# Optimization experiments

Measured on AMD Instinct MI355X. Metric: run time of the kernel, lower is better.

The kernel has to match this reference:

```python
import jax, jax.numpy as jnp
import numpy as np

B, L, S, E, H = 2, 2048, 2048, 1024, 16
D = E // H


def setup_inputs() -> dict:
    key = jax.random.key(0)
    ks = jax.random.split(key, 16)
    p = 0.02  # small init scale for weights
    return {
        "a": jax.random.normal(ks[0], (B, L, E), jnp.float32),
        "b": jax.random.normal(ks[1], (B, S, E), jnp.float32),
        "Wa_qk": jax.random.normal(ks[2], (E, E), jnp.float32) * p,
        "ba_qk": jax.random.normal(ks[3], (E,), jnp.float32) * p,
        "Wa_v": jax.random.normal(ks[4], (E, E), jnp.float32) * p,
        "ba_v": jax.random.normal(ks[5], (E,), jnp.float32) * p,
        "Wb_qk": jax.random.normal(ks[6], (E, E), jnp.float32) * p,
        "bb_qk": jax.random.normal(ks[7], (E,), jnp.float32) * p,
        "Wb_v": jax.random.normal(ks[8], (E, E), jnp.float32) * p,
        "bb_v": jax.random.normal(ks[9], (E,), jnp.float32) * p,
        "Wa_o": jax.random.normal(ks[10], (E, E), jnp.float32) * p,
        "ba_o": jax.random.normal(ks[11], (E,), jnp.float32) * p,
        "Wb_o": jax.random.normal(ks[12], (E, E), jnp.float32) * p,
        "bb_o": jax.random.normal(ks[13], (E,), jnp.float32) * p,
    }


def _heads(x, n, W, bias):
    # x: [B, N, E] -> projected and split to [B, H, N, D]
    y = x @ W + bias
    return y.reshape(B, n, H, D).transpose(0, 2, 1, 3)


def reference(a, b, Wa_qk, ba_qk, Wa_v, ba_v, Wb_qk, bb_qk, Wb_v, bb_v,
              Wa_o, ba_o, Wb_o, bb_o):
    aq = _heads(a, L, Wa_qk, ba_qk)   # [B,H,L,D]
    av = _heads(a, L, Wa_v, ba_v)     # [B,H,L,D]
    bq = _heads(b, S, Wb_qk, bb_qk)   # [B,H,S,D]
    bv = _heads(b, S, Wb_v, bb_v)     # [B,H,S,D]

    scale = 1.0 / jnp.sqrt(jnp.float32(D))
    # Shared score matrix [B,H,L,S]
    scores = jnp.einsum('bhld,bhsd->bhls', aq, bq) * scale
    # Dual softmax: row-wise (over S) and column-wise (over L)
    wa = jax.nn.softmax(scores, axis=-1)                    # [B,H,L,S]
    wb = jax.nn.softmax(scores, axis=-2).transpose(0, 1, 3, 2)  # [B,H,S,L]

    a_ctx = jnp.einsum('bhls,bhsd->bhld', wa, bv)  # [B,H,L,D]
    b_ctx = jnp.einsum('bhsl,bhld->bhsd', wb, av)  # [B,H,S,D]

    a_out = a_ctx.transpose(0, 2, 1, 3).reshape(B, L, E) @ Wa_o + ba_o
    b_out = b_ctx.transpose(0, 2, 1, 3).reshape(B, S, E) @ Wb_o + bb_o
    return (a_out, b_out)
```

## Files before the change

### kernel.cpp

```cpp
#include <hip/hip_runtime.h>
#include <hip/hip_bf16.h>
#include <stdint.h>

typedef unsigned short u16;
typedef unsigned int u32;
typedef __attribute__((ext_vector_type(8))) short bf16x8;
typedef __attribute__((ext_vector_type(4))) float f32x4;

typedef __attribute__((address_space(3))) void lds_void;
typedef const __attribute__((address_space(1))) void gbl_void;

#define SIDE 4194304u
#define BHSTR 131072u

static __device__ __forceinline__ u16 f2bf(float f) {
  union { __hip_bfloat16 b; u16 u; } cv;
  cv.b = __float2bfloat16(f);
  return cv.u;
}
static __device__ __forceinline__ float bf2f(u16 u) {
  union { __hip_bfloat16 b; u16 u; } cv;
  cv.u = u;
  return __bfloat162float(cv.b);
}

static __device__ __forceinline__ void pl16swap(u32& a, u32& b) {
#if __has_builtin(__builtin_amdgcn_permlane16_swap)
  typedef __attribute__((ext_vector_type(2))) unsigned int u32x2;
  u32x2 r = __builtin_amdgcn_permlane16_swap(a, b, 0, 0);
  a = r[0];
  b = r[1];
#else
  asm volatile("v_permlane16_swap_b32 %0, %1" : "+v"(a), "+v"(b));
#endif
}

__global__ __launch_bounds__(256) void k_cvt_in(const float* __restrict__ a,
                                                const float* __restrict__ b,
                                                u16* __restrict__ dst) {
  int z = blockIdx.y;
  const float* src = z ? b : a;
  size_t i = ((size_t)blockIdx.x * 256 + threadIdx.x) * 8;
  float4 x0 = *(const float4*)(src + i);
  float4 x1 = *(const float4*)(src + i + 4);
  u16 t[8] = {f2bf(x0.x), f2bf(x0.y), f2bf(x0.z), f2bf(x0.w),
              f2bf(x1.x), f2bf(x1.y), f2bf(x1.z), f2bf(x1.w)};
  *(uint4*)(dst + (size_t)z * SIDE + i) = *(uint4*)t;
}

__global__ __launch_bounds__(256) void k_cvt_bias(
    const float* s0, const float* s1, const float* s2, const float* s3,
    const float* s4, const float* s5, u16* __restrict__ dst) {
  const float* srcs[6] = {s0, s1, s2, s3, s4, s5};
  int z = blockIdx.y;
  int i = blockIdx.x * 256 + threadIdx.x;
  float sc = (z == 0) ? 0.18033688011112042f : 1.0f;
  dst[z * 1024 + i] = f2bf(srcs[z][i] * sc);
}

__global__ __launch_bounds__(256) void k_transpose_w(
    const float* a0, const float* a1, const float* a2, const float* a3,
    const float* a4, const float* a5,
    u16* d0, u16* d1, u16* d2, u16* d3, u16* d4, u16* d5) {
  __shared__ u16 tile[64][72];
  const float* srcs[6] = {a0, a1, a2, a3, a4, a5};
  u16* dsts[6] = {d0, d1, d2, d3, d4, d5};
  int z = blockIdx.z;
  float sc = (z == 0) ? 0.18033688011112042f : 1.0f;
  const float* src = srcs[z] + (size_t)(blockIdx.y * 64) * 1024 + blockIdx.x * 64;
  int t = threadIdx.x;
  int row = t >> 2, c4 = t & 3;
#pragma unroll
  for (int p = 0; p < 2; ++p) {
    int col = c4 * 8 + p * 32;
    const float* sf = src + (size_t)row * 1024 + col;
    float4 x0 = *(const float4*)sf;
    float4 x1 = *(const float4*)(sf + 4);
    u16 tmp[8] = {f2bf(x0.x * sc), f2bf(x0.y * sc), f2bf(x0.z * sc), f2bf(x0.w * sc),
                  f2bf(x1.x * sc), f2bf(x1.y * sc), f2bf(x1.z * sc), f2bf(x1.w * sc)};
    *(uint4*)(&tile[row][col]) = *(uint4*)tmp;
  }
  __syncthreads();
  u16* dst = dsts[z] + (size_t)(blockIdx.x * 64) * 1024 + blockIdx.y * 64;
#pragma unroll
  for (int p = 0; p < 2; ++p) {
    int col = c4 * 8 + p * 32;
    u16 tmp[8];
#pragma unroll
    for (int i = 0; i < 8; ++i) tmp[i] = tile[col + i][row];
    *(uint4*)(dst + (size_t)row * 1024 + col) = *(uint4*)tmp;
  }
}

__global__ __launch_bounds__(256) void k_gemm_qkv(
    const u16* __restrict__ Aall, const u16* __restrict__ WtA,
    const u16* __restrict__ WtB, const u16* __restrict__ bias,
    u16* __restrict__ qkbuf, u16* __restrict__ vbuf) {
  __shared__ u16 Sh[8192];
  u16* As = Sh;
  u16* Bs = Sh + 4096;
  int tid = threadIdx.x;
  int wave = tid >> 6, lane = tid & 63;
  int quad = lane >> 4, lrow = lane & 15;
  int wr = wave >> 1, wc = wave & 1;
  int z = blockIdx.z;
  int m0 = blockIdx.y * 128, n0 = blockIdx.x * 128;
  const u16* A = Aall + (size_t)z * SIDE;
  const u16* Wt = z ? WtB : WtA;
  const u16* bi = bias + (size_t)z * 2048;

  f32x4 acc[4][4] = {};
  int srow = 32 * wave + (lane >> 2);
  int scol = (lane & 3) * 8;
  const u16* gA = A + (size_t)(m0 + srow) * 1024 + scol;
  const u16* gB = Wt + (size_t)(n0 + srow) * 1024 + scol;
  u16* lA = &As[(32 * wave) * 32];
  u16* lB = &Bs[(32 * wave) * 32];

  for (int k0 = 0; k0 < 1024; k0 += 32) {
    __syncthreads();
#pragma unroll
    for (int j = 0; j < 2; ++j) {
      __builtin_amdgcn_global_load_lds((gbl_void*)(gA + (size_t)(16 * j) * 1024 + k0),
                                       (lds_void*)(lA + 16 * j * 32), 16, 0, 0);
      __builtin_amdgcn_global_load_lds((gbl_void*)(gB + (size_t)(16 * j) * 1024 + k0),
                                       (lds_void*)(lB + 16 * j * 32), 16, 0, 0);
    }
    __syncthreads();
    bf16x8 af[4], bfr[4];
#pragma unroll
    for (int i = 0; i < 4; ++i)
      af[i] = *(const bf16x8*)&As[(64 * wr + 16 * i + lrow) * 32 + 8 * quad];
#pragma unroll
    for (int j = 0; j < 4; ++j)
      bfr[j] = *(const bf16x8*)&Bs[(64 * wc + 16 * j + lrow) * 32 + 8 * quad];
#pragma unroll
    for (int i = 0; i < 4; ++i)
#pragma unroll
      for (int j = 0; j < 4; ++j)
        acc[i][j] = __builtin_amdgcn_mfma_f32_16x16x32_bf16(af[i], bfr[j], acc[i][j], 0, 0, 0);
  }

  float bv[4];
#pragma unroll
  for (int j = 0; j < 4; ++j) bv[j] = bf2f(bi[n0 + 64 * wc + 16 * j + lrow]);

  int x = blockIdx.x;
  bool isv = (x >= 8);
  int h = (isv ? 2 * (x - 8) : 2 * x) + wc;
  u16* dst = (isv ? vbuf : qkbuf) + (size_t)z * SIDE;
  u16* lw = Sh + wave * 1216;

  __syncthreads();
#pragma unroll
  for (int i = 0; i < 4; ++i) {
#pragma unroll
    for (int j = 0; j < 4; ++j)
#pragma unroll
      for (int r = 0; r < 4; ++r)
        lw[(4 * quad + r) * 76 + 16 * j + lrow] = f2bf(acc[i][j][r] + bv[j]);
    asm volatile("s_waitcnt lgkmcnt(0)" ::: "memory");
    int row = lane >> 2, cg = (lane & 3) * 16;
    int rg = m0 + 64 * wr + 16 * i + row;
    int bb = rg >> 11, rl = rg & 2047;
    u16* dr = dst + (size_t)(bb * 16 + h) * BHSTR + (size_t)rl * 64 + cg;
    uint2 w0 = *(const uint2*)&lw[row * 76 + cg];
    uint2 w1 = *(const uint2*)&lw[row * 76 + cg + 4];
    uint2 w2 = *(const uint2*)&lw[row * 76 + cg + 8];
    uint2 w3 = *(const uint2*)&lw[row * 76 + cg + 12];
    uint4 o0 = {w0.x, w0.y, w1.x, w1.y};
    uint4 o1 = {w2.x, w2.y, w3.x, w3.y};
    *(uint4*)dr = o0;
    *(uint4*)(dr + 8) = o1;
    asm volatile("s_waitcnt lgkmcnt(0)" ::: "memory");
  }
}

__global__ __launch_bounds__(256) void k_transpose_v(const u16* __restrict__ v,
                                                     u16* __restrict__ vt) {
  __shared__ u16 tile[64][72];
  int sbh = blockIdx.y;
  int n0 = blockIdx.x * 64;
  const u16* src = v + (size_t)sbh * BHSTR + (size_t)n0 * 64;
  u16* dst = vt + (size_t)sbh * BHSTR + n0;
  int t = threadIdx.x;
  int row = t >> 2, c4 = t & 3;
#pragma unroll
  for (int p = 0; p < 2; ++p) {
    int col = c4 * 8 + p * 32;
    uint4 q = *(const uint4*)(src + (size_t)row * 64 + col);
    *(uint4*)(&tile[row][col]) = q;
  }
  __syncthreads();
#pragma unroll
  for (int p = 0; p < 2; ++p) {
    int col = c4 * 8 + p * 32;
    u16 tmp[8];
#pragma unroll
    for (int i = 0; i < 8; ++i) tmp[i] = tile[col + i][row];
    *(uint4*)(dst + (size_t)row * 2048 + col) = *(uint4*)tmp;
  }
}

__global__ __launch_bounds__(256, 4) void k_attn(
    const u16* __restrict__ qk, const u16* __restrict__ vt,
    u16* __restrict__ ctx) {
  __shared__ u16 Ks[2 * 4096];
  __shared__ u16 Vs[2 * 4096];
  int tid = threadIdx.x;
  int wave = tid >> 6, lane = tid & 63;
  int quad = lane >> 4, lrow = lane & 15;
  int z = blockIdx.z, bh = blockIdx.x;
  int l0 = blockIdx.y * 128;
  const u16* Qb = qk + (size_t)z * SIDE + (size_t)bh * BHSTR + (size_t)l0 * 64;
  const u16* Kb = qk + (size_t)(1 - z) * SIDE + (size_t)bh * BHSTR;
  const u16* Vtb = vt + (size_t)(1 - z) * SIDE + (size_t)bh * BHSTR;

  bf16x8 qf[2][2];
#pragma unroll
  for (int rt = 0; rt < 2; ++rt) {
    int lq = 32 * wave + 16 * rt + lrow;
    qf[rt][0] = *(const bf16x8*)&Qb[(size_t)lq * 64 + 8 * quad];
    qf[rt][1] = *(const bf16x8*)&Qb[(size_t)lq * 64 + 32 + 8 * quad];
  }

  int r0 = tid >> 3, c0 = tid & 7;
  int r1 = (256 + tid) >> 3;
  const u16* kS0 = Kb + (size_t)r0 * 64 + ((c0 ^ (r0 & 7)) * 8);
  const u16* kS1 = Kb + (size_t)r1 * 64 + ((c0 ^ (r1 & 7)) * 8);
  const u16* vS0 = Vtb + (size_t)r0 * 2048 + ((c0 ^ (r0 & 7)) * 8);
  const u16* vS1 = Vtb + (size_t)r1 * 2048 + ((c0 ^ (r1 & 7)) * 8);
  u16* kD0 = Ks + (wave * 64) * 8;
  u16* kD1 = Ks + (256 + wave * 64) * 8;
  u16* vD0 = Vs + (wave * 64) * 8;
  u16* vD1 = Vs + (256 + wave * 64) * 8;

  bf16x8 ones;
  {
    short o = 0x3F80;
#pragma unroll
    for (int i = 0; i < 8; ++i) ones[i] = o;
  }

  f32x4 cacc[2][4] = {};
  f32x4 asum[2] = {};
  int gsq = 2 * (quad & 1) + (quad >> 1);

#define STAGE(BUFOFF, IT)                                                        \
  __builtin_amdgcn_global_load_lds((gbl_void*)(kS0 + (size_t)(IT)*4096),         \
                                   (lds_void*)(kD0 + (BUFOFF)), 16, 0, 0);       \
  __builtin_amdgcn_global_load_lds((gbl_void*)(kS1 + (size_t)(IT)*4096),         \
                                   (lds_void*)(kD1 + (BUFOFF)), 16, 0, 0);       \
  __builtin_amdgcn_global_load_lds((gbl_void*)(vS0 + (size_t)(IT)*64),           \
                                   (lds_void*)(vD0 + (BUFOFF)), 16, 0, 0);       \
  __builtin_amdgcn_global_load_lds((gbl_void*)(vS1 + (size_t)(IT)*64),           \
                                   (lds_void*)(vD1 + (BUFOFF)), 16, 0, 0);

#define ATT_BODY(BUFOFF)                                                         \
  {                                                                              \
    const u16* KsC = Ks + (BUFOFF);                                              \
    const u16* VsC = Vs + (BUFOFF);                                              \
    u32 X[2][4], Y[2][4];                                                        \
    _Pragma("unroll") for (int j = 0; j < 4; ++j) {                              \
      int kr = 16 * j + lrow;                                                    \
      bf16x8 kf0 = *(const bf16x8*)&KsC[(kr * 8 + (quad ^ (kr & 7))) * 8];       \
      bf16x8 kf1 = *(const bf16x8*)&KsC[(kr * 8 + ((quad + 4) ^ (kr & 7))) * 8]; \
      _Pragma("unroll") for (int rt = 0; rt < 2; ++rt) {                         \
        f32x4 s = {};                                                            \
        s = __builtin_amdgcn_mfma_f32_16x16x32_bf16(kf0, qf[rt][0], s, 0, 0, 0); \
        s = __builtin_amdgcn_mfma_f32_16x16x32_bf16(kf1, qf[rt][1], s, 0, 0, 0); \
        float e0 = exp2f(s[0]), e1 = exp2f(s[1]);                                \
        float e2 = exp2f(s[2]), e3 = exp2f(s[3]);                                \
        X[rt][j] = ((u32)f2bf(e1) << 16) | (u32)f2bf(e0);                        \
        Y[rt][j] = ((u32)f2bf(e3) << 16) | (u32)f2bf(e2);                        \
      }                                                                          \
    }                                                                            \
    bf16x8 pf[2][2];                                                             \
    _Pragma("unroll") for (int rt = 0; rt < 2; ++rt) {                           \
      pl16swap(X[rt][0], X[rt][1]);                                              \
      pl16swap(Y[rt][0], Y[rt][1]);                                              \
      pl16swap(X[rt][2], X[rt][3]);                                              \
      pl16swap(Y[rt][2], Y[rt][3]);                                              \
      union { u32 d[4]; bf16x8 v; } u0, u1;                                      \
      u0.d[0] = X[rt][0]; u0.d[1] = Y[rt][0];                                    \
      u0.d[2] = X[rt][1]; u0.d[3] = Y[rt][1];                                    \
      u1.d[0] = X[rt][2]; u1.d[1] = Y[rt][2];                                    \
      u1.d[2] = X[rt][3]; u1.d[3] = Y[rt][3];                                    \
      pf[rt][0] = u0.v;                                                          \
      pf[rt][1] = u1.v;                                                          \
    }                                                                            \
    _Pragma("unroll") for (int jd = 0; jd < 4; ++jd) {                           \
      int vr = 16 * jd + lrow;                                                   \
      bf16x8 vf0 = *(const bf16x8*)&VsC[(vr * 8 + (gsq ^ (vr & 7))) * 8];        \
      bf16x8 vf1 = *(const bf16x8*)&VsC[(vr * 8 + ((gsq | 4) ^ (vr & 7))) * 8];  \
      _Pragma("unroll") for (int rt = 0; rt < 2; ++rt) {                         \
        cacc[rt][jd] = __builtin_amdgcn_mfma_f32_16x16x32_bf16(pf[rt][0], vf0, cacc[rt][jd], 0, 0, 0); \
        cacc[rt][jd] = __builtin_amdgcn_mfma_f32_16x16x32_bf16(pf[rt][1], vf1, cacc[rt][jd], 0, 0, 0); \
      }                                                                          \
    }                                                                            \
    _Pragma("unroll") for (int rt = 0; rt < 2; ++rt) {                           \
      asum[rt] = __builtin_amdgcn_mfma_f32_16x16x32_bf16(pf[rt][0], ones, asum[rt], 0, 0, 0); \
      asum[rt] = __builtin_amdgcn_mfma_f32_16x16x32_bf16(pf[rt][1], ones, asum[rt], 0, 0, 0); \
    }                                                                            \
  }

  STAGE(0, 0)

  for (int it2 = 0; it2 < 16; ++it2) {
    int it = 2 * it2;
    __syncthreads();
    STAGE(4096, it + 1)
    ATT_BODY(0)
    __syncthreads();
    if (it2 < 15) {
      STAGE(0, it + 2)
    }
    ATT_BODY(4096)
  }
#undef ATT_BODY
#undef STAGE

  int bb = bh >> 4, h = bh & 15;
  u16* Ob = ctx + (size_t)z * SIDE + (size_t)(bb * 2048 + l0) * 1024 + h * 64;
#pragma unroll
  for (int rt = 0; rt < 2; ++rt) {
#pragma unroll
    for (int r = 0; r < 4; ++r) {
      float rinv = 1.0f / asum[rt][r];
      int l = 32 * wave + 16 * rt + 4 * quad + r;
#pragma unroll
      for (int j = 0; j < 4; ++j)
        Ob[(size_t)l * 1024 + 16 * j + lrow] = f2bf(cacc[rt][j][r] * rinv);
    }
  }
}

__global__ __launch_bounds__(256) void k_gemm_o(
    const u16* __restrict__ ctx, const u16* __restrict__ WtO,
    const u16* __restrict__ bias, float* __restrict__ out) {
  __shared__ u16 As[128 * 32];
  __shared__ u16 Bs[128 * 32];
  int tid = threadIdx.x;
  int wave = tid >> 6, lane = tid & 63;
  int quad = lane >> 4, lrow = lane & 15;
  int wr = wave >> 1, wc = wave & 1;
  int z = blockIdx.z;
  int m0 = blockIdx.y * 128, n0 = blockIdx.x * 128;
  const u16* A = ctx + (size_t)z * SIDE;
  const u16* Wt = WtO + (size_t)z * 1048576;
  const u16* bi = bias + (size_t)z * 1024;
  float* C = out + (size_t)z * SIDE;

  f32x4 acc[4][4] = {};
  int srow = 32 * wave + (lane >> 2);
  int scol = (lane & 3) * 8;
  const u16* gA = A + (size_t)(m0 + srow) * 1024 + scol;
  const u16* gB = Wt + (size_t)(n0 + srow) * 1024 + scol;
  u16* lA = &As[(32 * wave) * 32];
  u16* lB = &Bs[(32 * wave) * 32];

  for (int k0 = 0; k0 < 1024; k0 += 32) {
    __syncthreads();
#pragma unroll
    for (int j = 0; j < 2; ++j) {
      __builtin_amdgcn_global_load_lds((gbl_void*)(gA + (size_t)(16 * j) * 1024 + k0),
                                       (lds_void*)(lA + 16 * j * 32), 16, 0, 0);
      __builtin_amdgcn_global_load_lds((gbl_void*)(gB + (size_t)(16 * j) * 1024 + k0),
                                       (lds_void*)(lB + 16 * j * 32), 16, 0, 0);
    }
    __syncthreads();
    bf16x8 af[4], bfr[4];
#pragma unroll
    for (int i = 0; i < 4; ++i)
      af[i] = *(const bf16x8*)&As[(64 * wr + 16 * i + lrow) * 32 + 8 * quad];
#pragma unroll
    for (int j = 0; j < 4; ++j)
      bfr[j] = *(const bf16x8*)&Bs[(64 * wc + 16 * j + lrow) * 32 + 8 * quad];
#pragma unroll
    for (int i = 0; i < 4; ++i)
#pragma unroll
      for (int j = 0; j < 4; ++j)
        acc[i][j] = __builtin_amdgcn_mfma_f32_16x16x32_bf16(af[i], bfr[j], acc[i][j], 0, 0, 0);
  }

  float bv[4];
#pragma unroll
  for (int j = 0; j < 4; ++j) bv[j] = bf2f(bi[n0 + 64 * wc + 16 * j + lrow]);
#pragma unroll
  for (int i = 0; i < 4; ++i) {
    int row = m0 + 64 * wr + 16 * i + 4 * quad;
#pragma unroll
    for (int j = 0; j < 4; ++j) {
      int col = n0 + 64 * wc + 16 * j + lrow;
#pragma unroll
      for (int r = 0; r < 4; ++r)
        C[(size_t)(row + r) * 1024 + col] = acc[i][j][r] + bv[j];
    }
  }
}

extern "C" void kernel_launch(void* const* d_in, const int* in_sizes, int n_in,
                              void* d_out, int out_size, void* d_ws, size_t ws_size,
                              hipStream_t stream) {
  (void)in_sizes; (void)n_in; (void)out_size; (void)ws_size;
  const size_t M1 = 1048576u;
  u16* ws = (u16*)d_ws;
  u16* wtA   = ws;
  u16* wtB   = ws + 2 * M1;
  u16* wtO   = ws + 4 * M1;
  u16* biasQ = ws + 6 * M1;
  u16* biasO = ws + 6 * M1 + 4096;
  u16* ab    = ws + 7 * M1;
  u16* vt    = ab;
  u16* qkbuf = ws + 15 * M1;
  u16* vbuf  = ws + 23 * M1;
  u16* ctx   = vbuf;

  dim3 blk(256);
  k_cvt_in<<<dim3(2048, 2), blk, 0, stream>>>((const float*)d_in[0],
                                              (const float*)d_in[1], ab);
  k_cvt_bias<<<dim3(4, 6), blk, 0, stream>>>(
      (const float*)d_in[3], (const float*)d_in[5], (const float*)d_in[7],
      (const float*)d_in[9], (const float*)d_in[11], (const float*)d_in[13], biasQ);
  k_transpose_w<<<dim3(16, 16, 6), blk, 0, stream>>>(
      (const float*)d_in[2], (const float*)d_in[4], (const float*)d_in[6],
      (const float*)d_in[8], (const float*)d_in[10], (const float*)d_in[12],
      wtA, wtA + M1, wtB, wtB + M1, wtO, wtO + M1);
  k_gemm_qkv<<<dim3(16, 32, 2), blk, 0, stream>>>(ab, wtA, wtB, biasQ, qkbuf, vbuf);
  k_transpose_v<<<dim3(32, 64), blk, 0, stream>>>(vbuf, vt);
  k_attn<<<dim3(32, 16, 2), blk, 0, stream>>>(qkbuf, vt, ctx);
  k_gemm_o<<<dim3(8, 32, 2), blk, 0, stream>>>(ctx, wtO, biasO, (float*)d_out);
}
```

Measured before the change: 319.5 us.

## Double GEMM K-tile to 64 with XOR-swizzled LDS and use hardware exp2

Both projection GEMMs now stage 64-wide K tiles in LDS instead of 32-wide, halving the number of barrier pairs per K loop. The LDS layout gets an XOR swizzle on 16-byte chunks to avoid bank conflicts on the fragment reads. Separately, the attention kernel swaps exp2f for the raw v_exp_f32 intrinsic, dropping the denormal/range handling wrapper. The cost is doubled LDS per block, which may lower occupancy.

```diff
diff --git a/kernel.cpp b/kernel.cpp
--- a/kernel.cpp
+++ b/kernel.cpp
@@ -22,6 +22,16 @@
   union { __hip_bfloat16 b; u16 u; } cv;
   cv.u = u;
   return __bfloat162float(cv.b);
+}
+
+static __device__ __forceinline__ float fast_exp2(float x) {
+#if __has_builtin(__builtin_amdgcn_exp2f)
+  return __builtin_amdgcn_exp2f(x);
+#else
+  float r;
+  asm("v_exp_f32 %0, %1" : "=v"(r) : "v"(x));
+  return r;
+#endif
 }
 
 static __device__ __forceinline__ void pl16swap(u32& a, u32& b) {
@@ -96,9 +106,9 @@
     const u16* __restrict__ Aall, const u16* __restrict__ WtA,
     const u16* __restrict__ WtB, const u16* __restrict__ bias,
     u16* __restrict__ qkbuf, u16* __restrict__ vbuf) {
-  __shared__ u16 Sh[8192];
+  __shared__ u16 Sh[16384];
   u16* As = Sh;
-  u16* Bs = Sh + 4096;
+  u16* Bs = Sh + 8192;
   int tid = threadIdx.x;
   int wave = tid >> 6, lane = tid & 63;
   int quad = lane >> 4, lrow = lane & 15;
@@ -110,35 +120,39 @@
   const u16* bi = bias + (size_t)z * 2048;
 
   f32x4 acc[4][4] = {};
-  int srow = 32 * wave + (lane >> 2);
-  int scol = (lane & 3) * 8;
-  const u16* gA = A + (size_t)(m0 + srow) * 1024 + scol;
-  const u16* gB = Wt + (size_t)(n0 + srow) * 1024 + scol;
-  u16* lA = &As[(32 * wave) * 32];
-  u16* lB = &Bs[(32 * wave) * 32];
-
-  for (int k0 = 0; k0 < 1024; k0 += 32) {
-    __syncthreads();
-#pragma unroll
-    for (int j = 0; j < 2; ++j) {
-      __builtin_amdgcn_global_load_lds((gbl_void*)(gA + (size_t)(16 * j) * 1024 + k0),
-                                       (lds_void*)(lA + 16 * j * 32), 16, 0, 0);
-      __builtin_amdgcn_global_load_lds((gbl_void*)(gB + (size_t)(16 * j) * 1024 + k0),
-                                       (lds_void*)(lB + 16 * j * 32), 16, 0, 0);
-    }
-    __syncthreads();
-    bf16x8 af[4], bfr[4];
-#pragma unroll
-    for (int i = 0; i < 4; ++i)
-      af[i] = *(const bf16x8*)&As[(64 * wr + 16 * i + lrow) * 32 + 8 * quad];
-#pragma unroll
-    for (int j = 0; j < 4; ++j)
-      bfr[j] = *(const bf16x8*)&Bs[(64 * wc + 16 * j + lrow) * 32 + 8 * quad];
-#pragma unroll
-    for (int i = 0; i < 4; ++i)
+  int srow = 32 * wave + (lane >> 3);
+  int ssw = ((lane & 7) ^ (lane >> 3)) * 8;
+  const u16* gA = A + (size_t)(m0 + srow) * 1024 + ssw;
+  const u16* gB = Wt + (size_t)(n0 + srow) * 1024 + ssw;
+  u16* lA = &As[(32 * wave) * 64];
+  u16* lB = &Bs[(32 * wave) * 64];
+
+  for (int k0 = 0; k0 < 1024; k0 += 64) {
+    __syncthreads();
+#pragma unroll
+    for (int j = 0; j < 4; ++j) {
+      __builtin_amdgcn_global_load_lds((gbl_void*)(gA + (size_t)(8 * j) * 1024 + k0),
+                                       (lds_void*)(lA + 8 * j * 64), 16, 0, 0);
+      __builtin_amdgcn_global_load_lds((gbl_void*)(gB + (size_t)(8 * j) * 1024 + k0),
+                                       (lds_void*)(lB + 8 * j * 64), 16, 0, 0);
+    }
+    __syncthreads();
+#pragma unroll
+    for (int kk = 0; kk < 2; ++kk) {
+      int gq = ((kk << 2) + quad) ^ (lrow & 7);
+      bf16x8 af[4], bfr[4];
+#pragma unroll
+      for (int i = 0; i < 4; ++i)
+        af[i] = *(const bf16x8*)&As[(64 * wr + 16 * i + lrow) * 64 + gq * 8];
 #pragma unroll
       for (int j = 0; j < 4; ++j)
-        acc[i][j] = __builtin_amdgcn_mfma_f32_16x16x32_bf16(af[i], bfr[j], acc[i][j], 0, 0, 0);
+        bfr[j] = *(const bf16x8*)&Bs[(64 * wc + 16 * j + lrow) * 64 + gq * 8];
+#pragma unroll
+      for (int i = 0; i < 4; ++i)
+#pragma unroll
+        for (int j = 0; j < 4; ++j)
+          acc[i][j] = __builtin_amdgcn_mfma_f32_16x16x32_bf16(af[i], bfr[j], acc[i][j], 0, 0, 0);
+    }
   }
 
   float bv[4];
@@ -269,8 +283,8 @@
         f32x4 s = {};                                                            \
         s = __builtin_amdgcn_mfma_f32_16x16x32_bf16(kf0, qf[rt][0], s, 0, 0, 0); \
         s = __builtin_amdgcn_mfma_f32_16x16x32_bf16(kf1, qf[rt][1], s, 0, 0, 0); \
-        float e0 = exp2f(s[0]), e1 = exp2f(s[1]);                                \
-        float e2 = exp2f(s[2]), e3 = exp2f(s[3]);                                \
+        float e0 = fast_exp2(s[0]), e1 = fast_exp2(s[1]);                        \
+        float e2 = fast_exp2(s[2]), e3 = fast_exp2(s[3]);                        \
         X[rt][j] = ((u32)f2bf(e1) << 16) | (u32)f2bf(e0);                        \
         Y[rt][j] = ((u32)f2bf(e3) << 16) | (u32)f2bf(e2);                        \
       }                                                                          \
@@ -338,8 +352,8 @@
 __global__ __launch_bounds__(256) void k_gemm_o(
     const u16* __restrict__ ctx, const u16* __restrict__ WtO,
     const u16* __restrict__ bias, float* __restrict__ out) {
-  __shared__ u16 As[128 * 32];
-  __shared__ u16 Bs[128 * 32];
+  __shared__ u16 As[128 * 64];
+  __shared__ u16 Bs[128 * 64];
   int tid = threadIdx.x;
   int wave = tid >> 6, lane = tid & 63;
   int quad = lane >> 4, lrow = lane & 15;
@@ -352,35 +366,39 @@
   float* C = out + (size_t)z * SIDE;
 
   f32x4 acc[4][4] = {};
-  int srow = 32 * wave + (lane >> 2);
-  int scol = (lane & 3) * 8;
-  const u16* gA = A + (size_t)(m0 + srow) * 1024 + scol;
-  const u16* gB = Wt + (size_t)(n0 + srow) * 1024 + scol;
-  u16* lA = &As[(32 * wave) * 32];
-  u16* lB = &Bs[(32 * wave) * 32];
-
-  for (int k0 = 0; k0 < 1024; k0 += 32) {
-    __syncthreads();
-#pragma unroll
-    for (int j = 0; j < 2; ++j) {
-      __builtin_amdgcn_global_load_lds((gbl_void*)(gA + (size_t)(16 * j) * 1024 + k0),
-                                       (lds_void*)(lA + 16 * j * 32), 16, 0, 0);
-      __builtin_amdgcn_global_load_lds((gbl_void*)(gB + (size_t)(16 * j) * 1024 + k0),
-                                       (lds_void*)(lB + 16 * j * 32), 16, 0, 0);
-    }
-    __syncthreads();
-    bf16x8 af[4], bfr[4];
-#pragma unroll
-    for (int i = 0; i < 4; ++i)
-      af[i] = *(const bf16x8*)&As[(64 * wr + 16 * i + lrow) * 32 + 8 * quad];
-#pragma unroll
-    for (int j = 0; j < 4; ++j)
-      bfr[j] = *(const bf16x8*)&Bs[(64 * wc + 16 * j + lrow) * 32 + 8 * quad];
-#pragma unroll
-    for (int i = 0; i < 4; ++i)
+  int srow = 32 * wave + (lane >> 3);
+  int ssw = ((lane & 7) ^ (lane >> 3)) * 8;
+  const u16* gA = A + (size_t)(m0 + srow) * 1024 + ssw;
+  const u16* gB = Wt + (size_t)(n0 + srow) * 1024 + ssw;
+  u16* lA = &As[(32 * wave) * 64];
+  u16* lB = &Bs[(32 * wave) * 64];
+
+  for (int k0 = 0; k0 < 1024; k0 += 64) {
+    __syncthreads();
+#pragma unroll
+    for (int j = 0; j < 4; ++j) {
+      __builtin_amdgcn_global_load_lds((gbl_void*)(gA + (size_t)(8 * j) * 1024 + k0),
+                                       (lds_void*)(lA + 8 * j * 64), 16, 0, 0);
+      __builtin_amdgcn_global_load_lds((gbl_void*)(gB + (size_t)(8 * j) * 1024 + k0),
+                                       (lds_void*)(lB + 8 * j * 64), 16, 0, 0);
+    }
+    __syncthreads();
+#pragma unroll
+    for (int kk = 0; kk < 2; ++kk) {
+      int gq = ((kk << 2) + quad) ^ (lrow & 7);
+      bf16x8 af[4], bfr[4];
+#pragma unroll
+      for (int i = 0; i < 4; ++i)
+        af[i] = *(const bf16x8*)&As[(64 * wr + 16 * i + lrow) * 64 + gq * 8];
 #pragma unroll
       for (int j = 0; j < 4; ++j)
-        acc[i][j] = __builtin_amdgcn_mfma_f32_16x16x32_bf16(af[i], bfr[j], acc[i][j], 0, 0, 0);
+        bfr[j] = *(const bf16x8*)&Bs[(64 * wc + 16 * j + lrow) * 64 + gq * 8];
+#pragma unroll
+      for (int i = 0; i < 4; ++i)
+#pragma unroll
+        for (int j = 0; j < 4; ++j)
+          acc[i][j] = __builtin_amdgcn_mfma_f32_16x16x32_bf16(af[i], bfr[j], acc[i][j], 0, 0, 0);
+    }
   }
 
   float bv[4];
```

Result: faster. 276.1 us (-13.6%).
